# Optimization experiments

Hardware: AMD Instinct MI355X
Metric: run time of the kernel (lower is better)

## Reference

```python
import math
import jax, jax.numpy as jnp
import numpy as np

EMBED_DIM = 512
NUM_HEADS = 8
EDGE_VOC = 16
EDGE_PAD = 0
L, B = 512, 16


def setup_inputs() -> dict:
    key = jax.random.key(0)
    ks = jax.random.split(key, 8)
    x = jax.random.normal(ks[0], (L, B, EMBED_DIM), dtype=jnp.float32)
    edge = jax.random.randint(ks[1], (B, L, L), 0, EDGE_VOC, dtype=jnp.int32)
    key_padding_mask = jnp.zeros((B, L), dtype=bool)
    # causal additive mask, as from nn.Transformer.generate_square_subsequent_mask
    attn_mask = jnp.where(jnp.triu(jnp.ones((L, L), bool), k=1), -jnp.inf, 0.0).astype(jnp.float32)
    s = 1.0 / math.sqrt(EMBED_DIM)
    in_proj_w = jax.random.uniform(ks[2], (3 * EMBED_DIM, EMBED_DIM), jnp.float32, -s, s)
    in_proj_b = jnp.zeros((3 * EMBED_DIM,), jnp.float32)
    out_proj_w = jax.random.uniform(ks[3], (EMBED_DIM, EMBED_DIM), jnp.float32, -s, s)
    out_proj_b = jnp.zeros((EMBED_DIM,), jnp.float32)
    edge_emb = jax.random.normal(ks[4], (EDGE_VOC, NUM_HEADS), dtype=jnp.float32)
    edge_emb = edge_emb.at[EDGE_PAD].set(0.0)  # padding_idx row zeroed
    return {"x": x, "edge": edge, "key_padding_mask": key_padding_mask,
            "attn_mask": attn_mask, "in_proj_w": in_proj_w, "in_proj_b": in_proj_b,
            "out_proj_w": out_proj_w, "out_proj_b": out_proj_b, "edge_emb": edge_emb}


def reference(x, edge, key_padding_mask, attn_mask,
              in_proj_w, in_proj_b, out_proj_w, out_proj_b, edge_emb):
    length, bsz, embed_dim = x.shape
    H = edge_emb.shape[1]
    hd = embed_dim // H
    qkv = x @ in_proj_w.T + in_proj_b                       # (L, B, 3E)
    q, k, v = jnp.split(qkv, 3, axis=-1)
    # (L, B*H, hd) -> (B*H, L, hd)
    q = q.reshape(length, bsz * H, hd).transpose(1, 0, 2)
    k = k.reshape(length, bsz * H, hd).transpose(1, 0, 2)
    v = v.reshape(length, bsz * H, hd).transpose(1, 0, 2)
    # combine attn_mask with key padding
    mask = attn_mask[None]                                   # (1, L, L)
    kpm = jnp.broadcast_to(key_padding_mask[:, None, None, :],
                           (bsz, H, 1, length)).reshape(bsz * H, 1, length)
    mask = jnp.where(kpm, -jnp.inf, mask)                    # (B*H, 1/L, L)
    # edge bias: (B, L, L, H) -> (B*H, L, L)
    ebias = edge_emb[edge].transpose(0, 3, 1, 2).reshape(bsz * H, length, length)
    q = q / math.sqrt(hd)
    scores = jnp.einsum('bqd,bkd->bqk', q, k) + mask + ebias
    attn = jax.nn.softmax(scores, axis=-1)
    out = jnp.einsum('bqk,bkd->bqd', attn, v)                # (B*H, L, hd)
    out = out.transpose(1, 0, 2).reshape(length, bsz, embed_dim)
    return out @ out_proj_w.T + out_proj_b
```

## Files before the change

### kernel.cpp

```cpp
#include <hip/hip_runtime.h>
#include <hip/hip_bf16.h>


typedef __attribute__((ext_vector_type(8))) short bf16x8;
typedef __attribute__((ext_vector_type(4))) float f32x4;
typedef __attribute__((ext_vector_type(4))) int i32x4;

#define LOG2E 1.44269504088896340736f

__device__ inline void gll16(const void* g, const void* l) {
  __builtin_amdgcn_global_load_lds(
      (const __attribute__((address_space(1))) unsigned int*)g,
      (__attribute__((address_space(3))) unsigned int*)l, 16, 0, 0);
}

__device__ inline short f2bf(float x) {
  __hip_bfloat16 t = __float2bfloat16(x);
  return *reinterpret_cast<short*>(&t);
}

__device__ inline void cstore(__hip_bfloat16* C, size_t idx, float v) {
  C[idx] = __float2bfloat16(v);
}
__device__ inline void cstore(float* C, size_t idx, float v) { C[idx] = v; }

__global__ void cvt_pack(const float* __restrict__ x,
                         const float* __restrict__ w1,
                         const float* __restrict__ w2,
                         const int* __restrict__ edge,
                         __hip_bfloat16* __restrict__ xb,
                         __hip_bfloat16* __restrict__ w1b,
                         __hip_bfloat16* __restrict__ w2b,
                         unsigned int* __restrict__ epk) {
  const int blk = blockIdx.x;
  if (blk >= 2560) {
    const int t = (blk - 2560) * 256 + threadIdx.x;
    const int base = t * 8;
    const i32x4 a = *(const i32x4*)(edge + base);
    const i32x4 b = *(const i32x4*)(edge + base + 4);
    unsigned int w = 0;
#pragma unroll
    for (int j = 0; j < 4; j++) {
      w |= ((unsigned int)(a[j] & 15)) << (4 * j);
      w |= ((unsigned int)(b[j] & 15)) << (16 + 4 * j);
    }
    epk[t] = w;
    return;
  }
  const float* src;
  __hip_bfloat16* dst;
  int off;
  if (blk < 2048)      { src = x;  dst = xb;  off = blk; }
  else if (blk < 2432) { src = w1; dst = w1b; off = blk - 2048; }
  else                 { src = w2; dst = w2b; off = blk - 2432; }
  const int i = (off * 256 + threadIdx.x) * 8;
  const float4 a = *(const float4*)(src + i);
  const float4 b = *(const float4*)(src + i + 4);
  bf16x8 r;
  r[0] = f2bf(a.x); r[1] = f2bf(a.y); r[2] = f2bf(a.z); r[3] = f2bf(a.w);
  r[4] = f2bf(b.x); r[5] = f2bf(b.y); r[6] = f2bf(b.z); r[7] = f2bf(b.w);
  *(bf16x8*)(dst + i) = r;
}

template <int MT, typename TC>
__global__ __launch_bounds__(256, 2) void gemm_bt(
    const __hip_bfloat16* __restrict__ A,
    const __hip_bfloat16* __restrict__ W,
    const float* __restrict__ bias,
    TC* __restrict__ C, int N, int K) {
  constexpr int MI = MT / 32;
  __shared__ short As[MT * 32];
  __shared__ short Ws[128 * 32];
  const int tid = threadIdx.x;
  const int wave = tid >> 6, lane = tid & 63;
  const int c = lane & 15, quad = lane >> 4;
  const int nb = N >> 7;
  const int bx = blockIdx.x % nb, by = blockIdx.x / nb;
  const int m0 = by * MT, n0 = bx << 7;
  const int wm = wave >> 1, wn = wave & 1;

  f32x4 acc[MI][4] = {};
  const int ar = lane >> 2;
  const int ak = (lane & 3) * 8;

  for (int k0 = 0; k0 < K; k0 += 32) {
    __syncthreads();
#pragma unroll
    for (int i = 0; i < MT / 64; i++) {
      const int r0 = i * 64 + wave * 16;
      gll16(A + (size_t)(m0 + r0 + ar) * K + k0 + ak, &As[r0 * 32]);
    }
#pragma unroll
    for (int i = 0; i < 2; i++) {
      const int r0 = i * 64 + wave * 16;
      gll16(W + (size_t)(n0 + r0 + ar) * K + k0 + ak, &Ws[r0 * 32]);
    }
    __syncthreads();
    bf16x8 af[MI], bfr[4];
#pragma unroll
    for (int i = 0; i < MI; i++)
      af[i] = *(const bf16x8*)&As[(wm * (MT / 2) + i * 16 + c) * 32 + quad * 8];
#pragma unroll
    for (int j = 0; j < 4; j++)
      bfr[j] = *(const bf16x8*)&Ws[(wn * 64 + j * 16 + c) * 32 + quad * 8];
#pragma unroll
    for (int i = 0; i < MI; i++)
#pragma unroll
      for (int j = 0; j < 4; j++)
        acc[i][j] = __builtin_amdgcn_mfma_f32_16x16x32_bf16(af[i], bfr[j],
                                                            acc[i][j], 0, 0, 0);
  }
#pragma unroll
  for (int j = 0; j < 4; j++) {
    const int col = n0 + wn * 64 + j * 16 + c;
    const float bv = bias[col];
#pragma unroll
    for (int i = 0; i < MI; i++) {
      const int row = m0 + wm * (MT / 2) + i * 16 + quad * 4;
#pragma unroll
      for (int r = 0; r < 4; r++)
        cstore(C, (size_t)(row + r) * N + col, acc[i][j][r] + bv);
    }
  }
}

__global__ __launch_bounds__(256, 4) void attn_kernel(
    const __hip_bfloat16* __restrict__ qkv,
    const unsigned short* __restrict__ ep16,
    const float* __restrict__ edge_emb,
    __hip_bfloat16* __restrict__ attn_out) {
  __shared__ short Ks[64 * 72];
  __shared__ short Vt[64 * 72];
  __shared__ short Ps[4][16 * 72];
  __shared__ float eeS[16];

  const int tid = threadIdx.x;
  const int wave = tid >> 6, lane = tid & 63;
  const int c = lane & 15, quad = lane >> 4;
  const int i = blockIdx.x;
  constexpr int pi[8] = {0, 7, 1, 6, 2, 5, 3, 4};
  const int qb = pi[((i & 7) + (i >> 8)) & 7];
  const int bh = i >> 3;
  const int b = bh >> 3, h = bh & 7;
  const int colq = h * 64;

  if (tid < 16) eeS[tid] = (edge_emb[tid * 8 + h] - 16.0f) * LOG2E;

  const int q_g = (qb << 6) + wave * 16 + c;
  bf16x8 qf0, qf1;
  {
    const __hip_bfloat16* qp_ = qkv + (size_t)(q_g * 16 + b) * 1536 + colq;
    qf0 = *(const bf16x8*)(qp_ + quad * 8);
    qf1 = *(const bf16x8*)(qp_ + 32 + quad * 8);
  }
  float lsum = 0.f;
  f32x4 o[4] = {};
  const int enib = (b * 512 + q_g) * 512;

  __syncthreads();

  const int nkt = qb + 1;
  for (int kt = 0; kt < nkt; kt++) {
    const int k0 = kt << 6;
    if (kt) __syncthreads();
#pragma unroll
    for (int it = 0; it < 2; it++) {
      const int idx = it * 256 + tid;
      const int r = idx >> 3, cc = (idx & 7) * 8;
      const size_t base = (size_t)((k0 + r) * 16 + b) * 1536 + colq;
      *(bf16x8*)&Ks[r * 72 + cc] = *(const bf16x8*)(qkv + base + 512 + cc);
      const bf16x8 v = *(const bf16x8*)(qkv + base + 1024 + cc);
      const int kcol = (r & 7) | (((r >> 3) ^ (cc >> 3)) << 3);
#pragma unroll
      for (int j = 0; j < 8; j++) Vt[(cc + j) * 72 + kcol] = v[j];
    }
    unsigned int ew[4];
#pragma unroll
    for (int mt = 0; mt < 4; mt++)
      ew[mt] = ep16[(enib + k0 + mt * 16 + quad * 4) >> 2];
    __syncthreads();

    f32x4 st[4];
#pragma unroll
    for (int mt = 0; mt < 4; mt++) {
      const bf16x8 ka = *(const bf16x8*)&Ks[(mt * 16 + c) * 72 + quad * 8];
      const bf16x8 kb = *(const bf16x8*)&Ks[(mt * 16 + c) * 72 + 32 + quad * 8];
      f32x4 z = {0.f, 0.f, 0.f, 0.f};
      z = __builtin_amdgcn_mfma_f32_16x16x32_bf16(ka, qf0, z, 0, 0, 0);
      st[mt] = __builtin_amdgcn_mfma_f32_16x16x32_bf16(kb, qf1, z, 0, 0, 0);
    }
    float rsum = 0.0f;
#pragma unroll
    for (int mt = 0; mt < 4; mt++) {
      short4 pk;
#pragma unroll
      for (int r = 0; r < 4; r++) {
        const int key = k0 + mt * 16 + quad * 4 + r;
        const int code = (ew[mt] >> (4 * r)) & 15;
        const float p = (key <= q_g)
            ? exp2f(fmaf(st[mt][r], 0.125f * LOG2E, eeS[code]))
            : 0.0f;
        rsum += p;
        ((short*)&pk)[r] = f2bf(p);
      }
      *(short4*)&Ps[wave][c * 72 + mt * 16 + quad * 4] = pk;
    }
    lsum += rsum;
    const bf16x8 pa0 = *(const bf16x8*)&Ps[wave][c * 72 + quad * 8];
    const bf16x8 pa1 = *(const bf16x8*)&Ps[wave][c * 72 + 32 + quad * 8];
#pragma unroll
    for (int nt = 0; nt < 4; nt++) {
      const int n = nt * 16 + c;
      const bf16x8 vb0 = *(const bf16x8*)&Vt[n * 72 + ((quad ^ (n >> 3)) << 3)];
      const bf16x8 vb1 =
          *(const bf16x8*)&Vt[n * 72 + (((4 + quad) ^ (n >> 3)) << 3)];
      o[nt] = __builtin_amdgcn_mfma_f32_16x16x32_bf16(pa0, vb0, o[nt], 0, 0, 0);
      o[nt] = __builtin_amdgcn_mfma_f32_16x16x32_bf16(pa1, vb1, o[nt], 0, 0, 0);
    }
  }

  float l = lsum;
  l += __shfl_xor(l, 16);
  l += __shfl_xor(l, 32);
  float lr[4];
#pragma unroll
  for (int r = 0; r < 4; r++) lr[r] = __shfl(l, quad * 4 + r, 16);
  const int qrow0 = (qb << 6) + wave * 16 + quad * 4;
#pragma unroll
  for (int nt = 0; nt < 4; nt++)
#pragma unroll
    for (int r = 0; r < 4; r++)
      attn_out[(size_t)((qrow0 + r) * 16 + b) * 512 + colq + nt * 16 + c] =
          __float2bfloat16(o[nt][r] / lr[r]);
}

extern "C" void kernel_launch(void* const* d_in, const int* in_sizes, int n_in,
                              void* d_out, int out_size, void* d_ws, size_t ws_size,
                              hipStream_t stream) {
  const float* x    = (const float*)d_in[0];
  const int* edge   = (const int*)d_in[1];
  const float* ipw  = (const float*)d_in[4];
  const float* ipb  = (const float*)d_in[5];
  const float* opw  = (const float*)d_in[6];
  const float* opb  = (const float*)d_in[7];
  const float* eemb = (const float*)d_in[8];
  float* out = (float*)d_out;

  __hip_bfloat16* qkv  = (__hip_bfloat16*)d_ws;
  __hip_bfloat16* attn = qkv + (size_t)8192 * 1536;
  __hip_bfloat16* xb   = attn + (size_t)8192 * 512;
  __hip_bfloat16* w1b  = xb + (size_t)8192 * 512;
  __hip_bfloat16* w2b  = w1b + (size_t)1536 * 512;
  unsigned int* epk    = (unsigned int*)(w2b + (size_t)512 * 512);

  cvt_pack<<<4608, 256, 0, stream>>>(x, ipw, opw, edge, xb, w1b, w2b, epk);
  gemm_bt<128, __hip_bfloat16>
      <<<768, 256, 0, stream>>>(xb, w1b, ipb, qkv, 1536, 512);
  attn_kernel<<<1024, 256, 0, stream>>>(qkv, (const unsigned short*)epk, eemb,
                                        attn);
  gemm_bt<64, float>
      <<<512, 256, 0, stream>>>(attn, w2b, opb, out, 512, 512);
}
```

Measured before the change: 155.7 us.

## Prefetch next K/V tile into registers and pack V transpose stores

Loads the next key/value tile from global memory into registers while the current tile is being computed, so global latency overlaps the MFMA work instead of stalling before each tile. Each thread now handles two adjacent rows, which lets the V transpose into shared memory write packed 32-bit pairs instead of single 16-bit values. The cost is higher register pressure from holding four bf16x8 prefetch vectors, which could lower occupancy.

```diff
diff --git a/kernel.cpp b/kernel.cpp
--- a/kernel.cpp
+++ b/kernel.cpp
@@ -157,22 +157,37 @@
   f32x4 o[4] = {};
   const int enib = (b * 512 + q_g) * 512;
 
+  const int r2 = tid >> 3;
+  const int cc = (tid & 7) * 8;
+  const int kcol0 = ((r2 << 1) & 7) | (((r2 >> 2) ^ (cc >> 3)) << 3);
+  const size_t sbase0 = (size_t)((r2 * 2) * 16 + b) * 1536 + colq + cc;
+  bf16x8 kreg[2], vreg[2];
+  kreg[0] = *(const bf16x8*)(qkv + sbase0 + 512);
+  vreg[0] = *(const bf16x8*)(qkv + sbase0 + 1024);
+  kreg[1] = *(const bf16x8*)(qkv + sbase0 + 24576 + 512);
+  vreg[1] = *(const bf16x8*)(qkv + sbase0 + 24576 + 1024);
+
   __syncthreads();
 
   const int nkt = qb + 1;
   for (int kt = 0; kt < nkt; kt++) {
     const int k0 = kt << 6;
     if (kt) __syncthreads();
-#pragma unroll
-    for (int it = 0; it < 2; it++) {
-      const int idx = it * 256 + tid;
-      const int r = idx >> 3, cc = (idx & 7) * 8;
-      const size_t base = (size_t)((k0 + r) * 16 + b) * 1536 + colq;
-      *(bf16x8*)&Ks[r * 72 + cc] = *(const bf16x8*)(qkv + base + 512 + cc);
-      const bf16x8 v = *(const bf16x8*)(qkv + base + 1024 + cc);
-      const int kcol = (r & 7) | (((r >> 3) ^ (cc >> 3)) << 3);
-#pragma unroll
-      for (int j = 0; j < 8; j++) Vt[(cc + j) * 72 + kcol] = v[j];
+    *(bf16x8*)&Ks[(r2 * 2) * 72 + cc] = kreg[0];
+    *(bf16x8*)&Ks[(r2 * 2 + 1) * 72 + cc] = kreg[1];
+#pragma unroll
+    for (int j = 0; j < 8; j++) {
+      short2 p;
+      p.x = vreg[0][j];
+      p.y = vreg[1][j];
+      *(short2*)&Vt[(cc + j) * 72 + kcol0] = p;
+    }
+    if (kt + 1 < nkt) {
+      const size_t nb_ = sbase0 + (size_t)(kt + 1) * 64 * 24576;
+      kreg[0] = *(const bf16x8*)(qkv + nb_ + 512);
+      vreg[0] = *(const bf16x8*)(qkv + nb_ + 1024);
+      kreg[1] = *(const bf16x8*)(qkv + nb_ + 24576 + 512);
+      vreg[1] = *(const bf16x8*)(qkv + nb_ + 24576 + 1024);
     }
     unsigned int ew[4];
 #pragma unroll
```

New measurement: 155.7 us. About the same (-0.0%).
